# Kernel tuning notes

Hardware: AMD Instinct MI355X
Metric: run time of the kernel (lower is better)

## Reference

```python
import jax, jax.numpy as jnp
import numpy as np

NUM_REGIONS = 29
OUT = 7          # RoIAlign output size
SR = 2           # sampling_ratio
IMG = 1024.0     # input image H = W
LN_EPS = 1e-5


def _layernorm(x, g, b):
    mu = jnp.mean(x, axis=-1, keepdims=True)
    var = jnp.mean(jnp.square(x - mu), axis=-1, keepdims=True)
    return (x - mu) * jax.lax.rsqrt(var + LN_EPS) * g + b


def _roi_align(fm, rois):
    """torchvision roi_align (aligned=False), spatial_scale=1.0, sampling_ratio=SR.
    fm: [B,C,H,W], rois: [B,R,4] (x1,y1,x2,y2 in feature coords). -> [B,R,C,OUT,OUT]"""
    B, C, H, W = fm.shape
    x1, y1, x2, y2 = jnp.moveaxis(rois, -1, 0)            # each [B,R]
    roi_w = jnp.maximum(x2 - x1, 1.0)
    roi_h = jnp.maximum(y2 - y1, 1.0)
    bw = roi_w / OUT
    bh = roi_h / OUT
    # sub-bin offsets: (bin + (s+0.5)/SR) for bin in [0,OUT), s in [0,SR)
    off = jnp.arange(OUT, dtype=jnp.float32)[:, None] + (jnp.arange(SR, dtype=jnp.float32)[None, :] + 0.5) / SR  # [OUT,SR]
    py = y1[..., None, None] + off * bh[..., None, None]  # [B,R,OUT,SR]
    px = x1[..., None, None] + off * bw[..., None, None]  # [B,R,OUT,SR]
    y = py[:, :, :, :, None, None]                        # [B,R,OUT,SR,1,1]
    x = px[:, :, None, None, :, :]                        # [B,R,1,1,OUT,SR]
    valid = (y >= -1.0) & (y <= H) & (x >= -1.0) & (x <= W)
    yc = jnp.clip(y, 0.0, H - 1.0)
    xc = jnp.clip(x, 0.0, W - 1.0)
    y0 = jnp.floor(yc).astype(jnp.int32)
    x0 = jnp.floor(xc).astype(jnp.int32)
    y1i = jnp.minimum(y0 + 1, H - 1)
    x1i = jnp.minimum(x0 + 1, W - 1)
    ly = yc - y0
    lx = xc - x0
    hy = 1.0 - ly
    hx = 1.0 - lx
    gather = jax.vmap(lambda f, yy, xx: f[:, yy, xx])     # per image: [C,H,W] -> [C,...]
    v00 = gather(fm, y0, x0)                              # [B,C,R,OUT,SR,OUT,SR]
    v01 = gather(fm, y0, x1i)
    v10 = gather(fm, y1i, x0)
    v11 = gather(fm, y1i, x1i)
    w00 = (hy * hx)[:, None]
    w01 = (hy * lx)[:, None]
    w10 = (ly * hx)[:, None]
    w11 = (ly * lx)[:, None]
    val = w00 * v00 + w01 * v01 + w10 * v10 + w11 * v11
    val = jnp.where(valid[:, None], val, 0.0)
    pooled = val.mean(axis=(4, 6))                        # average over SRxSR samples -> [B,C,R,OUT,OUT]
    return jnp.transpose(pooled, (0, 2, 1, 3, 4))         # [B,R,C,OUT,OUT]


def setup_inputs() -> dict:
    key = jax.random.key(0)
    ks = jax.random.split(key, 8)
    B, N, C, Hf, Wf, FD = 32, 40, 256, 64, 64, 768
    D = C * OUT * OUT
    feature_maps = jax.random.normal(ks[0], (B, C, Hf, Wf), jnp.float32)
    xy = jax.random.uniform(ks[1], (B, N, 2), jnp.float32) * 900.0
    wh = jax.random.uniform(ks[2], (B, N, 2), jnp.float32) * 100.0 + 16.0
    boxes = jnp.concatenate([xy, xy + wh], axis=-1)       # valid x1,y1,x2,y2 in image coords
    scores = jax.random.uniform(ks[3], (B, N), jnp.float32)
    labels = jax.random.randint(ks[4], (B, N), 0, NUM_REGIONS + 1)
    return {
        'feature_maps': feature_maps,
        'boxes': boxes,
        'scores': scores,
        'labels': labels,
        'w1': jax.random.normal(ks[5], (D, 2048), jnp.float32) * 0.02,
        'b1': jnp.zeros((2048,), jnp.float32),
        'g1': jnp.ones((2048,), jnp.float32),
        'be1': jnp.zeros((2048,), jnp.float32),
        'w2': jax.random.normal(ks[6], (2048, FD), jnp.float32) * 0.02,
        'b2': jnp.zeros((FD,), jnp.float32),
        'g2': jnp.ones((FD,), jnp.float32),
        'be2': jnp.zeros((FD,), jnp.float32),
        'missing_token': jax.random.normal(ks[7], (FD,), jnp.float32),
    }


def reference(feature_maps, boxes, scores, labels, w1, b1, g1, be1, w2, b2, g2, be2, missing_token):
    B, C, Hf, Wf = feature_maps.shape
    R = NUM_REGIONS
    scale = jnp.minimum(Hf / IMG, Wf / IMG)               # scale_factors (same for all images)
    # segmented argmax: best-scoring box per (image, region)
    region_idx = jnp.clip(labels, 1, R) - 1               # [B,N]
    onehot = region_idx[..., None] == jnp.arange(R)       # [B,N,R]
    masked = jnp.where(onehot, scores[..., None], -1.0)   # init best score = -1.0
    detected = jnp.any(onehot, axis=1)                    # [B,R]
    best = jnp.argmax(masked, axis=1)                     # [B,R] first max, matches strict-> loop
    sel = jnp.take_along_axis(boxes, jnp.broadcast_to(best[:, :, None], (B, R, 4)), axis=1)
    rois = sel * scale                                    # [B,R,4] in feature-map coords
    roi_feats = _roi_align(feature_maps, rois)            # [B,R,C,7,7]
    flat = roi_feats.reshape(B * R, C * OUT * OUT)
    h = _layernorm(flat @ w1 + b1, g1, be1)
    h = jax.nn.relu(h)
    h = _layernorm(h @ w2 + b2, g2, be2)                  # [B*R, feature_dim]
    feats = h.reshape(B, R, -1)
    region_features = jnp.where(detected[..., None], feats, missing_token)
    return region_features, detected
```

## Files before the change

kernel.cpp:

```cpp
#include <hip/hip_runtime.h>

typedef __bf16 bf16x8 __attribute__((ext_vector_type(8)));
typedef float f32x4 __attribute__((ext_vector_type(4)));
typedef unsigned short ushort8v __attribute__((ext_vector_type(8)));
typedef unsigned short ushort4v __attribute__((ext_vector_type(4)));

#define BATCH 32
#define NBOX 40
#define CCH 256
#define HF 64
#define WF 64
#define RREG 29
#define OUTP 7
#define MROWS 928
#define DDIM 12544
#define N1DIM 2048
#define FDIM 768
#define PDIM 4096
#define S1 7
#define S2 8

static constexpr size_t OFF_ROIS = 0;
static constexpr size_t OFF_DET  = 16384;
static constexpr size_t OFF_A    = 32768;
static constexpr size_t OFF_W1T  = OFF_A   + (size_t)MROWS * DDIM * 2;
static constexpr size_t OFF_W2T  = OFF_W1T + (size_t)DDIM * N1DIM * 2;
static constexpr size_t OFF_GP   = OFF_W2T + (size_t)N1DIM * FDIM * 2;
static constexpr size_t OFF_FMT  = OFF_GP  + (size_t)S1 * MROWS * N1DIM * 4;
static constexpr size_t OFF_H    = OFF_W1T;

static __device__ __forceinline__ unsigned short f2bf(float f) {
  __bf16 h = (__bf16)f;
  return __builtin_bit_cast(unsigned short, h);
}
static __device__ __forceinline__ float bf2f(unsigned short u) {
  unsigned int x = ((unsigned int)u) << 16;
  return __builtin_bit_cast(float, x);
}
static __device__ __forceinline__ void gload_lds16(const void* g, void* l) {
  __builtin_amdgcn_global_load_lds((const __attribute__((address_space(1))) void*)g,
                                   (__attribute__((address_space(3))) void*)l, 16, 0, 0);
}

__global__ __launch_bounds__(256) void selfmt_kernel(const float* __restrict__ in,
                                                     unsigned short* __restrict__ out,
                                                     const float* __restrict__ boxes,
                                                     const float* __restrict__ scores,
                                                     const int* __restrict__ labels,
                                                     float* __restrict__ rois,
                                                     int* __restrict__ det,
                                                     float* __restrict__ out_det) {
  __shared__ float tile[64][65];
  int bid = blockIdx.x;
  int t = threadIdx.x;
  if (bid >= PDIM / 64 * (CCH / 64) * BATCH) {
    int tid = (bid - PDIM / 64 * (CCH / 64) * BATCH) * 256 + t;
    if (tid >= MROWS) return;
    int b = tid / RREG, r = tid % RREG;
    float bestS = -1.0f;
    int bestN = 0;
    int found = 0;
    for (int n = 0; n < NBOX; ++n) {
      int lab = labels[b * NBOX + n];
      int ri = min(max(lab, 1), RREG) - 1;
      if (ri == r) {
        found = 1;
        float s = scores[b * NBOX + n];
        if (s > bestS) { bestS = s; bestN = n; }
      }
    }
    const float scale = 0.0625f;
    float4 bx = *(const float4*)&boxes[(b * NBOX + bestN) * 4];
    rois[tid * 4 + 0] = bx.x * scale;
    rois[tid * 4 + 1] = bx.y * scale;
    rois[tid * 4 + 2] = bx.z * scale;
    rois[tid * 4 + 3] = bx.w * scale;
    det[tid] = found;
    out_det[tid] = found ? 1.0f : 0.0f;
    return;
  }
  int p0 = (bid & 63) * 64, c0 = ((bid >> 6) & 3) * 64, b = bid >> 8;
  int tx = t & 15, ty = t >> 4;
#pragma unroll
  for (int q = 0; q < 4; ++q) {
    int r = ty + q * 16;
    float4 v = *(const float4*)&in[((long)b * CCH + c0 + r) * PDIM + p0 + tx * 4];
    tile[r][tx * 4 + 0] = v.x;
    tile[r][tx * 4 + 1] = v.y;
    tile[r][tx * 4 + 2] = v.z;
    tile[r][tx * 4 + 3] = v.w;
  }
  __syncthreads();
#pragma unroll
  for (int q = 0; q < 4; ++q) {
    int r = ty + q * 16;
    ushort4v o;
    o[0] = f2bf(tile[tx * 4 + 0][r]);
    o[1] = f2bf(tile[tx * 4 + 1][r]);
    o[2] = f2bf(tile[tx * 4 + 2][r]);
    o[3] = f2bf(tile[tx * 4 + 3][r]);
    *(ushort4v*)&out[((long)b * PDIM + p0 + r) * CCH + c0 + tx * 4] = o;
  }
}

__global__ __launch_bounds__(256) void roiwT_kernel(const unsigned short* __restrict__ fmT,
                                                    const float* __restrict__ rois,
                                                    unsigned short* __restrict__ A,
                                                    const float* __restrict__ w1,
                                                    unsigned short* __restrict__ w1t,
                                                    const float* __restrict__ w2,
                                                    unsigned short* __restrict__ w2t) {
  __shared__ __align__(16) char lds[31360];
  int bid = blockIdx.x;
  int t = threadIdx.x;

  if (bid < MROWS) {
    unsigned short* Arow = (unsigned short*)lds;
    int (*sidx)[4] = (int(*)[4])(lds + 25088);
    float (*swt)[4] = (float(*)[4])(lds + 28224);
    int roi = bid;
    float rx1 = rois[roi * 4 + 0], ry1 = rois[roi * 4 + 1];
    float rx2 = rois[roi * 4 + 2], ry2 = rois[roi * 4 + 3];
    float roiw = fmaxf(rx2 - rx1, 1.f), roih = fmaxf(ry2 - ry1, 1.f);
    float bw = roiw * (1.f / OUTP), bh = roih * (1.f / OUTP);
    if (t < 196) {
      int oy = t / 28, rem = t % 28, ox = rem / 4, s = rem % 4, sy = s >> 1, sx = s & 1;
      float y = ry1 + ((float)oy + ((float)sy + 0.5f) * 0.5f) * bh;
      float x = rx1 + ((float)ox + ((float)sx + 0.5f) * 0.5f) * bw;
      bool valid = (y >= -1.f) && (y <= 64.f) && (x >= -1.f) && (x <= 64.f);
      float yc = fminf(fmaxf(y, 0.f), 63.f);
      float xc = fminf(fmaxf(x, 0.f), 63.f);
      int y0 = (int)floorf(yc), x0 = (int)floorf(xc);
      int y1i = min(y0 + 1, 63), x1i = min(x0 + 1, 63);
      float ly = yc - (float)y0, lx = xc - (float)x0;
      float hy = 1.f - ly, hx = 1.f - lx;
      float m = valid ? 1.f : 0.f;
      swt[t][0] = hy * hx * m;
      swt[t][1] = hy * lx * m;
      swt[t][2] = ly * hx * m;
      swt[t][3] = ly * lx * m;
      sidx[t][0] = (y0 * 64 + x0) * CCH;
      sidx[t][1] = (y0 * 64 + x1i) * CCH;
      sidx[t][2] = (y1i * 64 + x0) * CCH;
      sidx[t][3] = (y1i * 64 + x1i) * CCH;
    }
    __syncthreads();
    int b = roi / RREG;
    int cg = t & 63;
    int sub = t >> 6;
    int start = sub * 12 + min(sub, 1);
    int cnt = sub == 0 ? 13 : 12;
    const unsigned short* base = fmT + (long)b * PDIM * CCH + cg * 4;
    for (int bi = 0; bi < cnt; ++bi) {
      int bin = start + bi;
      float a0 = 0.f, a1 = 0.f, a2 = 0.f, a3 = 0.f;
#pragma unroll
      for (int s = 0; s < 4; ++s) {
        int sid = bin * 4 + s;
#pragma unroll
        for (int tp = 0; tp < 4; ++tp) {
          float w = swt[sid][tp];
          ushort4v v = *(const ushort4v*)(base + sidx[sid][tp]);
          a0 += w * bf2f(v[0]);
          a1 += w * bf2f(v[1]);
          a2 += w * bf2f(v[2]);
          a3 += w * bf2f(v[3]);
        }
      }
      Arow[(cg * 4 + 0) * 49 + bin] = f2bf(a0 * 0.25f);
      Arow[(cg * 4 + 1) * 49 + bin] = f2bf(a1 * 0.25f);
      Arow[(cg * 4 + 2) * 49 + bin] = f2bf(a2 * 0.25f);
      Arow[(cg * 4 + 3) * 49 + bin] = f2bf(a3 * 0.25f);
    }
    __syncthreads();
    const ushort8v* src = (const ushort8v*)Arow;
    ushort8v* dst = (ushort8v*)(A + (long)roi * DDIM);
    for (int i = t; i < DDIM / 8; i += 256) dst[i] = src[i];
    return;
  }

  float (*tile)[65] = (float(*)[65])lds;
  int wb = bid - MROWS;
  const float* in;
  unsigned short* out;
  int K, N, k0, n0;
  if (wb < (DDIM / 64) * (N1DIM / 64)) {
    in = w1; out = w1t; K = DDIM; N = N1DIM;
    k0 = (wb % (DDIM / 64)) * 64;
    n0 = (wb / (DDIM / 64)) * 64;
  } else {
    int r = wb - (DDIM / 64) * (N1DIM / 64);
    in = w2; out = w2t; K = N1DIM; N = FDIM;
    k0 = (r % (N1DIM / 64)) * 64;
    n0 = (r / (N1DIM / 64)) * 64;
  }
  int tx = t & 15, ty = t >> 4;
#pragma unroll
  for (int p = 0; p < 4; ++p) {
    int r = ty + p * 16;
    float4 v = *(const float4*)&in[(long)(k0 + r) * N + n0 + tx * 4];
    tile[r][tx * 4 + 0] = v.x;
    tile[r][tx * 4 + 1] = v.y;
    tile[r][tx * 4 + 2] = v.z;
    tile[r][tx * 4 + 3] = v.w;
  }
  __syncthreads();
#pragma unroll
  for (int p = 0; p < 4; ++p) {
    int r = ty + p * 16;
    ushort4v o;
    o[0] = f2bf(tile[tx * 4 + 0][r]);
    o[1] = f2bf(tile[tx * 4 + 1][r]);
    o[2] = f2bf(tile[tx * 4 + 2][r]);
    o[3] = f2bf(tile[tx * 4 + 3][r]);
    *(ushort4v*)&out[(long)(n0 + r) * K + k0 + tx * 4] = o;
  }
}

__global__ __launch_bounds__(512, 2) void gemm1_8p_kernel(const unsigned short* __restrict__ A,
                                                          const unsigned short* __restrict__ Bt,
                                                          float* __restrict__ Cp) {
  __shared__ __align__(16) char lds[131072];
  int bid = blockIdx.x;
  int tile = (bid & 7) * 28 + (bid >> 3);
  int bm = tile & 3;
  int bn = (tile >> 2) & 7;
  int s = tile >> 5;
  long kb = (long)s * 1792;

  int t = threadIdx.x;
  int lane = t & 63, wv = t >> 6;
  int wr = wv >> 2, wc = wv & 3;
  int fr = lane & 15, fq = lane >> 4;
  int srow = t >> 3, sch = t & 7;

  f32x4 acc[8][4];
#pragma unroll
  for (int m = 0; m < 8; ++m)
#pragma unroll
    for (int n = 0; n < 4; ++n) acc[m][n] = (f32x4){0.f, 0.f, 0.f, 0.f};

#define STG(isB, h, ktl, bufs) do {                                            \
    _Pragma("unroll")                                                          \
    for (int j = 0; j < 2; ++j) {                                              \
      int rl = (h) * 128 + srow + j * 64;                                      \
      long grow = (isB) ? (long)(bn * 256 + rl) : (long)min(bm * 256 + rl, MROWS - 1); \
      const unsigned short* sp = ((isB) ? Bt : A) + grow * DDIM + kb + (ktl) * 64 \
                                 + ((sch ^ (rl & 7)) * 8);                     \
      gload_lds16(sp, lds + ((isB) ? 65536 : 0) + (bufs) * 32768               \
                          + (h) * 16384 + j * 8192 + t * 16);                  \
    }                                                                          \
  } while (0)

  STG(0, 0, 0, 0);
  STG(0, 1, 0, 0);
  STG(1, 0, 0, 0);
  STG(1, 1, 0, 0);
  asm volatile("s_waitcnt vmcnt(0)" ::: "memory");
  __builtin_amdgcn_sched_barrier(0);
  __builtin_amdgcn_s_barrier();
  __builtin_amdgcn_sched_barrier(0);

  for (int it = 0; it < 14; ++it) {
#pragma unroll
    for (int ph = 0; ph < 8; ++ph) {
      const int half = ph >> 2;
      const int q = ph & 3, mh = q >> 1, nh = q & 1;
      const int bufc = half, bufs = half ^ 1;

      bf16x8 af[4][2], bfv[2][2];
#pragma unroll
      for (int mi = 0; mi < 4; ++mi) {
        int row = wr * 128 + (mh * 4 + mi) * 16 + fr;
#pragma unroll
        for (int ks = 0; ks < 2; ++ks)
          af[mi][ks] = *(const bf16x8*)(lds + bufc * 32768 + row * 128
                                        + ((ks * 64 + fq * 16) ^ ((row & 7) << 4)));
      }
#pragma unroll
      for (int ni = 0; ni < 2; ++ni) {
        int row = wc * 64 + (nh * 2 + ni) * 16 + fr;
#pragma unroll
        for (int ks = 0; ks < 2; ++ks)
          bfv[ni][ks] = *(const bf16x8*)(lds + 65536 + bufc * 32768 + row * 128
                                         + ((ks * 64 + fq * 16) ^ ((row & 7) << 4)));
      }

      {
        int ktl = min(2 * it + 1 + half, 27);
        const int op = ph & 3;
        if (op == 0) STG(0, 0, ktl, bufs);
        else if (op == 1) STG(0, 1, ktl, bufs);
        else if (op == 2) STG(1, 0, ktl, bufs);
        else STG(1, 1, ktl, bufs);
      }

      if (ph == 3 || ph == 7) {
        asm volatile("s_waitcnt vmcnt(0)" ::: "memory");
        __builtin_amdgcn_sched_barrier(0);
      }
      __builtin_amdgcn_s_barrier();
      __builtin_amdgcn_sched_barrier(0);
      asm volatile("s_waitcnt lgkmcnt(0)" ::: "memory");
      __builtin_amdgcn_sched_barrier(0);

      __builtin_amdgcn_s_setprio(1);
#pragma unroll
      for (int mi = 0; mi < 4; ++mi)
#pragma unroll
        for (int ni = 0; ni < 2; ++ni)
#pragma unroll
          for (int ks = 0; ks < 2; ++ks)
            acc[mh * 4 + mi][nh * 2 + ni] = __builtin_amdgcn_mfma_f32_16x16x32_bf16(
                af[mi][ks], bfv[ni][ks], acc[mh * 4 + mi][nh * 2 + ni], 0, 0, 0);
      __builtin_amdgcn_s_setprio(0);
      __builtin_amdgcn_sched_barrier(0);
      __builtin_amdgcn_s_barrier();
      __builtin_amdgcn_sched_barrier(0);
    }
  }
#undef STG

  float* Cb = Cp + (long)s * MROWS * N1DIM;
#pragma unroll
  for (int m = 0; m < 8; ++m)
#pragma unroll
    for (int n = 0; n < 4; ++n) {
      int col = bn * 256 + wc * 64 + n * 16 + fr;
#pragma unroll
      for (int j = 0; j < 4; ++j) {
        int row = bm * 256 + wr * 128 + m * 16 + fq * 4 + j;
        if (row < MROWS) Cb[(long)row * N1DIM + col] = acc[m][n][j];
      }
    }
}

__global__ __launch_bounds__(256, 2) void gemm_sk_kernel(const unsigned short* __restrict__ A,
                                                         const unsigned short* __restrict__ Bt,
                                                         float* __restrict__ Cp,
                                                         int M, int N, int K, int kchunk,
                                                         int gy, int q) {
  __shared__ unsigned short As[2 * 128 * 64];
  __shared__ unsigned short Bs[2 * 128 * 64];
  int bid = blockIdx.x;
  int tile = (bid & 7) * q + (bid >> 3);
  int bm = tile & 7;
  int rest = tile >> 3;
  int bn = rest % gy;
  int s = rest / gy;

  int t = threadIdx.x;
  int lane = t & 63, wv = t >> 6;
  int wr = wv >> 1, wc = wv & 1;
  int fr = lane & 15, fq = lane >> 4;

  f32x4 acc[4][4];
#pragma unroll
  for (int m = 0; m < 4; ++m)
#pragma unroll
    for (int n = 0; n < 4; ++n) acc[m][n] = (f32x4){0.f, 0.f, 0.f, 0.f};

  int srow = t >> 3;
  int scol = t & 7;
  int k_begin = s * kchunk;
  int k_end = min(k_begin + kchunk, K);
  int nkt = (k_end - k_begin) >> 6;

  int garow[4], gbrow[4], schunk[4];
#pragma unroll
  for (int i = 0; i < 4; ++i) {
    int row = srow + i * 32;
    schunk[i] = (scol ^ (row & 7)) * 8;
    garow[i] = min(bm * 128 + row, M - 1);
    gbrow[i] = bn * 128 + row;
  }

#define GSTAGE(buf, kt_) do {                                                  \
    int k0_ = k_begin + (kt_) * 64;                                            \
    _Pragma("unroll")                                                          \
    for (int i = 0; i < 4; ++i)                                                \
      gload_lds16(A + (long)garow[i] * K + k0_ + schunk[i],                    \
                  (char*)As + (buf) * 16384 + t * 16 + i * 4096);              \
    _Pragma("unroll")                                                          \
    for (int i = 0; i < 4; ++i)                                                \
      gload_lds16(Bt + (long)gbrow[i] * K + k0_ + schunk[i],                   \
                  (char*)Bs + (buf) * 16384 + t * 16 + i * 4096);              \
  } while (0)

  GSTAGE(0, 0);
  GSTAGE(1, min(1, nkt - 1));

  for (int kt = 0; kt < nkt; ++kt) {
    int cur = kt & 1;
    asm volatile("s_waitcnt vmcnt(8)" ::: "memory");
    __builtin_amdgcn_sched_barrier(0);
    __builtin_amdgcn_s_barrier();
    __builtin_amdgcn_sched_barrier(0);

    const char* Ab = (const char*)As + cur * 16384;
    const char* Bb = (const char*)Bs + cur * 16384;
#pragma unroll
    for (int ks = 0; ks < 2; ++ks) {
      bf16x8 af[4], bfv2[4];
#pragma unroll
      for (int m = 0; m < 4; ++m) {
        int row = wr * 64 + m * 16 + fr;
        int bc = (ks * 64 + fq * 16) ^ ((row & 7) << 4);
        af[m] = *(const bf16x8*)(Ab + row * 128 + bc);
      }
#pragma unroll
      for (int n = 0; n < 4; ++n) {
        int row = wc * 64 + n * 16 + fr;
        int bc = (ks * 64 + fq * 16) ^ ((row & 7) << 4);
        bfv2[n] = *(const bf16x8*)(Bb + row * 128 + bc);
      }
#pragma unroll
      for (int m = 0; m < 4; ++m)
#pragma unroll
        for (int n = 0; n < 4; ++n)
          acc[m][n] = __builtin_amdgcn_mfma_f32_16x16x32_bf16(af[m], bfv2[n], acc[m][n], 0, 0, 0);
    }

    __builtin_amdgcn_sched_barrier(0);
    __builtin_amdgcn_s_barrier();
    __builtin_amdgcn_sched_barrier(0);
    GSTAGE(cur, min(kt + 2, nkt - 1));
  }
#undef GSTAGE

  float* Cb = Cp + (long)s * M * N;
#pragma unroll
  for (int m = 0; m < 4; ++m)
#pragma unroll
    for (int n = 0; n < 4; ++n) {
      int col = bn * 128 + wc * 64 + n * 16 + fr;
#pragma unroll
      for (int j = 0; j < 4; ++j) {
        int row = bm * 128 + wr * 64 + m * 16 + fq * 4 + j;
        if (row < M) Cb[(long)row * N + col] = acc[m][n][j];
      }
    }
}

static __device__ __forceinline__ void block_reduce2(float& a, float& b, float* sm) {
#pragma unroll
  for (int off = 32; off > 0; off >>= 1) {
    a += __shfl_down(a, off);
    b += __shfl_down(b, off);
  }
  int lane = threadIdx.x & 63, wv = threadIdx.x >> 6;
  if (lane == 0) { sm[wv] = a; sm[wv + 4] = b; }
  __syncthreads();
  a = sm[0] + sm[1] + sm[2] + sm[3];
  b = sm[4] + sm[5] + sm[6] + sm[7];
}

__global__ __launch_bounds__(256) void ln1_kernel(const float* __restrict__ X,
                                                  const float* __restrict__ b1,
                                                  const float* __restrict__ g1,
                                                  const float* __restrict__ be1,
                                                  unsigned short* __restrict__ H) {
  __shared__ float sm[8];
  int row = blockIdx.x, t = threadIdx.x;
  float x[8];
  float sum = 0.f, sq = 0.f;
#pragma unroll
  for (int i = 0; i < 8; ++i) {
    int j = t + i * 256;
    float v = b1[j];
#pragma unroll
    for (int s = 0; s < S1; ++s) v += X[((long)s * MROWS + row) * N1DIM + j];
    x[i] = v;
    sum += v;
    sq += v * v;
  }
  block_reduce2(sum, sq, sm);
  float mu = sum * (1.f / N1DIM);
  float inv = rsqrtf(sq * (1.f / N1DIM) - mu * mu + 1e-5f);
#pragma unroll
  for (int i = 0; i < 8; ++i) {
    int j = t + i * 256;
    float y = fmaxf((x[i] - mu) * inv * g1[j] + be1[j], 0.f);
    H[(long)row * N1DIM + j] = f2bf(y);
  }
}

__global__ __launch_bounds__(256) void ln2_kernel(const float* __restrict__ X,
                                                  const float* __restrict__ b2,
                                                  const float* __restrict__ g2,
                                                  const float* __restrict__ be2,
                                                  const float* __restrict__ miss,
                                                  const int* __restrict__ det,
                                                  float* __restrict__ out) {
  __shared__ float sm[8];
  int row = blockIdx.x, t = threadIdx.x;
  float x[3];
  float sum = 0.f, sq = 0.f;
#pragma unroll
  for (int i = 0; i < 3; ++i) {
    int j = t + i * 256;
    float v = b2[j];
#pragma unroll
    for (int s = 0; s < S2; ++s) v += X[((long)s * MROWS + row) * FDIM + j];
    x[i] = v;
    sum += v;
    sq += v * v;
  }
  block_reduce2(sum, sq, sm);
  float mu = sum * (1.f / FDIM);
  float inv = rsqrtf(sq * (1.f / FDIM) - mu * mu + 1e-5f);
  int dv = det[row];
#pragma unroll
  for (int i = 0; i < 3; ++i) {
    int j = t + i * 256;
    float y = (x[i] - mu) * inv * g2[j] + be2[j];
    out[(long)row * FDIM + j] = dv ? y : miss[j];
  }
}

extern "C" void kernel_launch(void* const* d_in, const int* in_sizes, int n_in,
                              void* d_out, int out_size, void* d_ws, size_t ws_size,
                              hipStream_t stream) {
  const float* fm     = (const float*)d_in[0];
  const float* boxes  = (const float*)d_in[1];
  const float* scores = (const float*)d_in[2];
  const int*   labels = (const int*)d_in[3];
  const float* w1     = (const float*)d_in[4];
  const float* b1     = (const float*)d_in[5];
  const float* g1     = (const float*)d_in[6];
  const float* be1    = (const float*)d_in[7];
  const float* w2     = (const float*)d_in[8];
  const float* b2     = (const float*)d_in[9];
  const float* g2     = (const float*)d_in[10];
  const float* be2    = (const float*)d_in[11];
  const float* miss   = (const float*)d_in[12];
  float* out = (float*)d_out;
  char* ws = (char*)d_ws;

  float* rois = (float*)(ws + OFF_ROIS);
  int* det = (int*)(ws + OFF_DET);
  unsigned short* Abf = (unsigned short*)(ws + OFF_A);
  unsigned short* fmT = (unsigned short*)(ws + OFF_FMT);
  unsigned short* w1t = (unsigned short*)(ws + OFF_W1T);
  unsigned short* w2t = (unsigned short*)(ws + OFF_W2T);
  float* Gp = (float*)(ws + OFF_GP);
  unsigned short* Hbf = (unsigned short*)(ws + OFF_H);

  hipLaunchKernelGGL(selfmt_kernel, dim3(8192 + 4), dim3(256), 0, stream,
                     fm, fmT, boxes, scores, labels, rois, det, out + (long)MROWS * FDIM);
  hipLaunchKernelGGL(roiwT_kernel,
                     dim3(MROWS + (DDIM / 64) * (N1DIM / 64) + (N1DIM / 64) * (FDIM / 64)),
                     dim3(256), 0, stream, fmT, rois, Abf, w1, w1t, w2, w2t);
  hipLaunchKernelGGL(gemm1_8p_kernel, dim3(224), dim3(512), 0, stream, Abf, w1t, Gp);
  hipLaunchKernelGGL(ln1_kernel, dim3(MROWS), dim3(256), 0, stream, Gp, b1, g1, be1, Hbf);
  {
    int nkb = N1DIM / 64;
    int kc = ((nkb + S2 - 1) / S2) * 64;
    int gy = FDIM / 128, nwg = 8 * gy * S2;
    hipLaunchKernelGGL(gemm_sk_kernel, dim3(nwg), dim3(256), 0, stream,
                       Hbf, w2t, Gp, MROWS, FDIM, N1DIM, kc, gy, nwg / 8);
  }
  hipLaunchKernelGGL(ln2_kernel, dim3(MROWS), dim3(256), 0, stream,
                     Gp, b2, g2, be2, miss, det, out);
}
```

Measured before the change: 189.6 us.

## Rebalance GEMM1 split-K to 256 workgroups and loosen its LDS pipeline barriers

```diff
diff --git a/kernel.cpp b/kernel.cpp
--- a/kernel.cpp
+++ b/kernel.cpp
@@ -17,7 +17,7 @@
 #define N1DIM 2048
 #define FDIM 768
 #define PDIM 4096
-#define S1 7
+#define S1 8
 #define S2 8
 
 static constexpr size_t OFF_ROIS = 0;
@@ -222,15 +222,16 @@
                                                           float* __restrict__ Cp) {
   __shared__ __align__(16) char lds[131072];
   int bid = blockIdx.x;
-  int tile = (bid & 7) * 28 + (bid >> 3);
+  int tile = (bid & 7) * 32 + (bid >> 3);
   int bm = tile & 3;
   int bn = (tile >> 2) & 7;
   int s = tile >> 5;
-  long kb = (long)s * 1792;
+  int nkt = (s < 7) ? 25 : 21;
+  long kb = (long)s * 1600;
 
   int t = threadIdx.x;
   int lane = t & 63, wv = t >> 6;
-  int wr = wv >> 2, wc = wv & 3;
+  int wr = (wv >> 2) & 1, wc = wv & 3;
   int fr = lane & 15, fq = lane >> 4;
   int srow = t >> 3, sch = t & 7;
 
@@ -253,25 +254,27 @@
   } while (0)
 
   STG(0, 0, 0, 0);
-  STG(0, 1, 0, 0);
   STG(1, 0, 0, 0);
   STG(1, 1, 0, 0);
-  asm volatile("s_waitcnt vmcnt(0)" ::: "memory");
-  __builtin_amdgcn_sched_barrier(0);
-  __builtin_amdgcn_s_barrier();
-  __builtin_amdgcn_sched_barrier(0);
-
-  for (int it = 0; it < 14; ++it) {
-#pragma unroll
-    for (int ph = 0; ph < 8; ++ph) {
-      const int half = ph >> 2;
-      const int q = ph & 3, mh = q >> 1, nh = q & 1;
-      const int bufc = half, bufs = half ^ 1;
+  STG(0, 1, 0, 0);
+
+  for (int H = 0; H < nkt; ++H) {
+    int bufc = H & 1, bufs = bufc ^ 1;
+    int ktn = min(H + 1, nkt - 1);
+#pragma unroll
+    for (int q = 0; q < 4; ++q) {
+      if (q < 3) {
+        asm volatile("s_waitcnt vmcnt(4)" ::: "memory");
+        __builtin_amdgcn_sched_barrier(0);
+        __builtin_amdgcn_s_barrier();
+        __builtin_amdgcn_sched_barrier(0);
+      }
+      const int mh = q >> 1, nh = q & 1;
 
       bf16x8 af[4][2], bfv[2][2];
 #pragma unroll
       for (int mi = 0; mi < 4; ++mi) {
-        int row = wr * 128 + (mh * 4 + mi) * 16 + fr;
+        int row = mh * 128 + wr * 64 + mi * 16 + fr;
 #pragma unroll
         for (int ks = 0; ks < 2; ++ks)
           af[mi][ks] = *(const bf16x8*)(lds + bufc * 32768 + row * 128
@@ -279,31 +282,20 @@
       }
 #pragma unroll
       for (int ni = 0; ni < 2; ++ni) {
-        int row = wc * 64 + (nh * 2 + ni) * 16 + fr;
+        int row = nh * 128 + wc * 32 + ni * 16 + fr;
 #pragma unroll
         for (int ks = 0; ks < 2; ++ks)
           bfv[ni][ks] = *(const bf16x8*)(lds + 65536 + bufc * 32768 + row * 128
                                          + ((ks * 64 + fq * 16) ^ ((row & 7) << 4)));
       }
 
-      {
-        int ktl = min(2 * it + 1 + half, 27);
-        const int op = ph & 3;
-        if (op == 0) STG(0, 0, ktl, bufs);
-        else if (op == 1) STG(0, 1, ktl, bufs);
-        else if (op == 2) STG(1, 0, ktl, bufs);
-        else STG(1, 1, ktl, bufs);
-      }
-
-      if (ph == 3 || ph == 7) {
-        asm volatile("s_waitcnt vmcnt(0)" ::: "memory");
-        __builtin_amdgcn_sched_barrier(0);
-      }
-      __builtin_amdgcn_s_barrier();
-      __builtin_amdgcn_sched_barrier(0);
+      if (q == 0) STG(0, 0, ktn, bufs);
+      else if (q == 1) STG(1, 0, ktn, bufs);
+      else if (q == 2) STG(1, 1, ktn, bufs);
+      else STG(0, 1, ktn, bufs);
+
       asm volatile("s_waitcnt lgkmcnt(0)" ::: "memory");
       __builtin_amdgcn_sched_barrier(0);
-
       __builtin_amdgcn_s_setprio(1);
 #pragma unroll
       for (int mi = 0; mi < 4; ++mi)
@@ -315,21 +307,20 @@
                 af[mi][ks], bfv[ni][ks], acc[mh * 4 + mi][nh * 2 + ni], 0, 0, 0);
       __builtin_amdgcn_s_setprio(0);
       __builtin_amdgcn_sched_barrier(0);
-      __builtin_amdgcn_s_barrier();
-      __builtin_amdgcn_sched_barrier(0);
     }
   }
 #undef STG
+  asm volatile("s_waitcnt vmcnt(0) lgkmcnt(0)" ::: "memory");
 
   float* Cb = Cp + (long)s * MROWS * N1DIM;
 #pragma unroll
   for (int m = 0; m < 8; ++m)
 #pragma unroll
     for (int n = 0; n < 4; ++n) {
-      int col = bn * 256 + wc * 64 + n * 16 + fr;
+      int col = bn * 256 + (n >> 1) * 128 + wc * 32 + (n & 1) * 16 + fr;
 #pragma unroll
       for (int j = 0; j < 4; ++j) {
-        int row = bm * 256 + wr * 128 + m * 16 + fq * 4 + j;
+        int row = bm * 256 + (m >> 2) * 128 + wr * 64 + (m & 3) * 16 + fq * 4 + j;
         if (row < MROWS) Cb[(long)row * N1DIM + col] = acc[m][n][j];
       }
     }
@@ -551,7 +542,7 @@
   hipLaunchKernelGGL(roiwT_kernel,
                      dim3(MROWS + (DDIM / 64) * (N1DIM / 64) + (N1DIM / 64) * (FDIM / 64)),
                      dim3(256), 0, stream, fmT, rois, Abf, w1, w1t, w2, w2t);
-  hipLaunchKernelGGL(gemm1_8p_kernel, dim3(224), dim3(512), 0, stream, Abf, w1t, Gp);
+  hipLaunchKernelGGL(gemm1_8p_kernel, dim3(256), dim3(512), 0, stream, Abf, w1t, Gp);
   hipLaunchKernelGGL(ln1_kernel, dim3(MROWS), dim3(256), 0, stream, Gp, b1, g1, be1, Hbf);
   {
     int nkb = N1DIM / 64;
```

New measurement: 173.8 us. 8.4% less time.
